# Optimization experiments

Measured on AMD Instinct MI355X. Metric: run time of the kernel, lower is better.

Reference implementation:

```python
import math
import jax, jax.numpy as jnp
import numpy as np

NQ = 4   # n_qubits
NL = 2   # n_layers
H = 16   # num_heads


def _apply_gate(state, gate, q, batched):
    """Apply a 1-qubit gate on wire q to batched state [N, 2**NQ]."""
    n = state.shape[0]
    left, right = 2 ** q, 2 ** (NQ - 1 - q)
    s = state.reshape(n, left, 2, right)
    eq = 'nab,nlbr->nlar' if batched else 'ab,nlbr->nlar'
    return jnp.einsum(eq, gate, s).reshape(n, 2 ** NQ)


def _rot(phi, theta, omega):
    """PennyLane Rot(phi, theta, omega) = RZ(omega) RY(theta) RZ(phi), 2x2 unitary."""
    c = jnp.cos(theta / 2).astype(jnp.complex64)
    s = jnp.sin(theta / 2).astype(jnp.complex64)
    ep = jnp.exp(-0.5j * (phi + omega).astype(jnp.complex64))
    em = jnp.exp(0.5j * (phi - omega).astype(jnp.complex64))
    m00 = ep * c
    m01 = -em * s
    m10 = jnp.conj(em) * s
    m11 = jnp.conj(ep) * c
    return jnp.stack([jnp.stack([m00, m01]), jnp.stack([m10, m11])])


def _cnot01(state):
    """CNOT with control wire 0, target wire 1 on [N, 16]."""
    n = state.shape[0]
    s = state.reshape(n, 2, 2, 2 ** (NQ - 2))
    s = jnp.stack([s[:, 0], s[:, 1, ::-1]], axis=1)
    return s.reshape(n, 2 ** NQ)


def _quantum_block(inputs, params):
    """Analytic state-vector simulation of the PennyLane circuit.

    inputs: [N, NQ] rotation angles (AngleEmbedding, default RX).
    params: [NL, NQ, 3] Rot parameters.
    Returns [N, NQ] Pauli-Z expectation values.
    """
    n = inputs.shape[0]
    state = jnp.zeros((n, 2 ** NQ), jnp.complex64).at[:, 0].set(1.0)
    # AngleEmbedding: RX(inputs[:, q]) on wire q
    for q in range(NQ):
        a = inputs[:, q] * 0.5
        c = jnp.cos(a).astype(jnp.complex64)
        s = (-1j) * jnp.sin(a).astype(jnp.complex64)
        gate = jnp.stack([jnp.stack([c, s], -1), jnp.stack([s, c], -1)], -2)  # [N,2,2]
        state = _apply_gate(state, gate, q, batched=True)
    # Variational layers
    for l in range(NL):
        for q in range(NQ):
            g = _rot(params[l, q, 0], params[l, q, 1], params[l, q, 2])
            state = _apply_gate(state, g, q, batched=False)
        state = _cnot01(state)
    probs = (jnp.abs(state) ** 2).reshape(n, 2, 2, 2, 2)
    z = jnp.array([1.0, -1.0], probs.dtype)
    letters = 'abcd'
    evs = [jnp.einsum(f'nabcd,{letters[i]}->n', probs, z) for i in range(NQ)]
    return jnp.stack(evs, axis=-1)


def reference(x, params, w_q, w_k, w_v, w_o):
    B, S, E = x.shape
    dk = E // H

    def proj(w):
        return (x @ w.T).reshape(B, S, H, dk).transpose(0, 2, 1, 3)  # [B,H,S,dk]

    q, k, v = proj(w_q), proj(w_k), proj(w_v)

    def inject(t):
        ang = t[..., :NQ].reshape(-1, NQ)
        ev = _quantum_block(ang, params).reshape(B, H, S, NQ).astype(t.dtype)
        return t.at[..., :NQ].set(ev)

    q, k, v = inject(q), inject(k), inject(v)
    scores = jnp.einsum('bhqd,bhkd->bhqk', q, k) / math.sqrt(dk)
    attn = jax.nn.softmax(scores, axis=-1)
    out = jnp.einsum('bhqk,bhkd->bhqd', attn, v)
    out = out.transpose(0, 2, 1, 3).reshape(B, S, E)
    return out @ w_o.T


def setup_inputs() -> dict:
    key = jax.random.key(0)
    ks = jax.random.split(key, 6)
    B, S, E = 2, 2048, 1024
    scale = 1.0 / math.sqrt(E)
    return {
        'x': jax.random.normal(ks[0], (B, S, E), jnp.float32),
        'params': jax.random.normal(ks[1], (NL, NQ, 3), jnp.float32),
        'w_q': jax.random.normal(ks[2], (E, E), jnp.float32) * scale,
        'w_k': jax.random.normal(ks[3], (E, E), jnp.float32) * scale,
        'w_v': jax.random.normal(ks[4], (E, E), jnp.float32) * scale,
        'w_o': jax.random.normal(ks[5], (E, E), jnp.float32) * scale,
    }
```

## Files before the change

### kernel.cpp

```cpp
#include <hip/hip_runtime.h>
#include <math.h>

#define BATCH 2
#define S_LEN 2048
#define E_DIM 1024
#define NHEAD 16
#define DK 64
#define NROWS (BATCH * S_LEN)

typedef _Float16 f16x8 __attribute__((ext_vector_type(8)));
typedef _Float16 f16x4 __attribute__((ext_vector_type(4)));
typedef float    f32x4 __attribute__((ext_vector_type(4)));

__global__ __launch_bounds__(256) void conv_all(
    const float* __restrict__ x,  const float* __restrict__ wq,
    const float* __restrict__ wk, const float* __restrict__ wv,
    const float* __restrict__ wo,
    _Float16* __restrict__ xh,  _Float16* __restrict__ wqh,
    _Float16* __restrict__ wkh, _Float16* __restrict__ wvh,
    _Float16* __restrict__ woh) {
    const int id = blockIdx.x;
    const float* src; _Float16* dst; int lid;
    if (id < 4096)      { src = x;  dst = xh;  lid = id; }
    else if (id < 5120) { src = wq; dst = wqh; lid = id - 4096; }
    else if (id < 6144) { src = wk; dst = wkh; lid = id - 5120; }
    else if (id < 7168) { src = wv; dst = wvh; lid = id - 6144; }
    else                { src = wo; dst = woh; lid = id - 7168; }
    const int i = lid * 256 + threadIdx.x;
    float4 v = ((const float4*)src)[i];
    f16x4 h;
    h[0] = (_Float16)v.x; h[1] = (_Float16)v.y;
    h[2] = (_Float16)v.z; h[3] = (_Float16)v.w;
    ((f16x4*)dst)[i] = h;
}

__device__ __forceinline__ void gemm_body(const _Float16* __restrict__ X,
                                          const _Float16* __restrict__ W,
                                          void* __restrict__ dstv, int mode,
                                          _Float16* smem) {
    _Float16* Xs = smem;
    _Float16* Ws = smem + 128 * 72;

    const int tid  = threadIdx.x;
    const int lane = tid & 63;
    const int wv   = tid >> 6;
    const int wy = wv >> 1, wx = wv & 1;
    const int l15 = lane & 15, quad = lane >> 4;
    const int m0 = blockIdx.y * 128, c0 = blockIdx.x * 128;

    const int srow = tid >> 3;
    const int skc  = (tid & 7) * 8;

    f32x4 acc[4][4];
#pragma unroll
    for (int i = 0; i < 4; ++i)
#pragma unroll
        for (int j = 0; j < 4; ++j) acc[i][j] = 0.f;

    for (int k0 = 0; k0 < E_DIM; k0 += 64) {
        f16x8 xg[4], wg[4];
#pragma unroll
        for (int c = 0; c < 4; ++c) {
            const int row = c * 32 + srow;
            xg[c] = *(const f16x8*)(X + (size_t)(m0 + row) * E_DIM + k0 + skc);
            wg[c] = *(const f16x8*)(W + (size_t)(c0 + row) * E_DIM + k0 + skc);
        }
        __syncthreads();
#pragma unroll
        for (int c = 0; c < 4; ++c) {
            const int row = c * 32 + srow;
            *(f16x8*)&Xs[row * 72 + skc] = xg[c];
            *(f16x8*)&Ws[row * 72 + skc] = wg[c];
        }
        __syncthreads();
#pragma unroll
        for (int ks = 0; ks < 2; ++ks) {
            f16x8 af[4], bf[4];
#pragma unroll
            for (int i = 0; i < 4; ++i) {
                af[i] = *(const f16x8*)&Xs[(wy * 64 + i * 16 + l15) * 72 + ks * 32 + quad * 8];
                bf[i] = *(const f16x8*)&Ws[(wx * 64 + i * 16 + l15) * 72 + ks * 32 + quad * 8];
            }
#pragma unroll
            for (int i = 0; i < 4; ++i)
#pragma unroll
                for (int j = 0; j < 4; ++j)
                    acc[i][j] = __builtin_amdgcn_mfma_f32_16x16x32_f16(af[i], bf[j], acc[i][j], 0, 0, 0);
        }
    }

    if (mode == 2) {
        __syncthreads();
        _Float16* Ct = smem;
#pragma unroll
        for (int i = 0; i < 4; ++i)
#pragma unroll
            for (int j = 0; j < 4; ++j) {
                const int col  = wx * 64 + j * 16 + l15;
                const int rowb = wy * 64 + i * 16 + quad * 4;
                f16x4 pk;
#pragma unroll
                for (int r = 0; r < 4; ++r) pk[r] = (_Float16)acc[i][j][r];
                *(f16x4*)&Ct[col * 136 + rowb] = pk;
            }
        __syncthreads();
        const int b  = m0 >> 11;
        const int s0 = m0 & 2047;
#pragma unroll
        for (int it = 0; it < 8; ++it) {
            const int c   = it * 256 + tid;
            const int col = c >> 4;
            const int rc  = c & 15;
            f16x8 v = *(const f16x8*)&Ct[col * 136 + rc * 8];
            const int e = c0 + col, h = e >> 6, d = e & 63;
            *(f16x8*)((_Float16*)dstv + ((size_t)((b * NHEAD + h) * DK + d)) * S_LEN + s0 + rc * 8) = v;
        }
        return;
    }

#pragma unroll
    for (int i = 0; i < 4; ++i)
#pragma unroll
        for (int j = 0; j < 4; ++j)
#pragma unroll
            for (int r = 0; r < 4; ++r) {
                const int row = m0 + wy * 64 + i * 16 + quad * 4 + r;
                const int col = c0 + wx * 64 + j * 16 + l15;
                if (mode == 0) {
                    ((float*)dstv)[(size_t)row * E_DIM + col] = acc[i][j][r];
                } else {
                    const int b = row >> 11, s = row & 2047;
                    const int h = col >> 6,  d = col & 63;
                    ((_Float16*)dstv)[(((size_t)(b * NHEAD + h) * S_LEN + s) * DK) + d] =
                        (_Float16)acc[i][j][r];
                }
            }
}

__global__ __launch_bounds__(256) void gemm_qkv(
    const _Float16* __restrict__ X,
    const _Float16* __restrict__ WQ, const _Float16* __restrict__ WK,
    const _Float16* __restrict__ WV,
    _Float16* __restrict__ Qh, _Float16* __restrict__ Kh,
    _Float16* __restrict__ VTh) {
    __shared__ __align__(16) _Float16 smem[2 * 128 * 72];
    const int z = blockIdx.z;
    const _Float16* W = (z == 0) ? WQ : (z == 1) ? WK : WV;
    void* dst = (z == 0) ? (void*)Qh : (z == 1) ? (void*)Kh : (void*)VTh;
    gemm_body(X, W, dst, (z == 2) ? 2 : 1, smem);
}

__global__ __launch_bounds__(256) void gemm_out(const _Float16* __restrict__ X,
                                                const _Float16* __restrict__ W,
                                                float* __restrict__ dst) {
    __shared__ __align__(16) _Float16 smem[2 * 128 * 72];
    gemm_body(X, W, dst, 0, smem);
}

__device__ __forceinline__ void apply_gate(float ar[16], float ai[16], int stride,
                                           float g00r, float g00i, float g01r, float g01i,
                                           float g10r, float g10i, float g11r, float g11i) {
#pragma unroll
    for (int i0 = 0; i0 < 16; ++i0) {
        if (i0 & stride) continue;
        const int i1 = i0 + stride;
        const float s0r = ar[i0], s0i = ai[i0];
        const float s1r = ar[i1], s1i = ai[i1];
        ar[i0] = g00r * s0r - g00i * s0i + g01r * s1r - g01i * s1i;
        ai[i0] = g00r * s0i + g00i * s0r + g01r * s1i + g01i * s1r;
        ar[i1] = g10r * s0r - g10i * s0i + g11r * s1r - g11i * s1i;
        ai[i1] = g10r * s0i + g10i * s0r + g11r * s1i + g11i * s1r;
    }
}

__global__ __launch_bounds__(256) void quantum_inject(_Float16* __restrict__ Q,
                                                      _Float16* __restrict__ K,
                                                      _Float16* __restrict__ VT,
                                                      const float* __restrict__ params) {
    const int id = blockIdx.x * 256 + threadIdx.x;
    const int which = id >> 16;
    const int rem = id & 65535;

    float angv[4];
    _Float16* qkbase = nullptr;
    _Float16* vbase  = nullptr;
    if (which == 2) {
        const int bh = rem >> 11, s = rem & 2047;
        vbase = VT + ((size_t)bh * DK) * S_LEN + s;
#pragma unroll
        for (int d = 0; d < 4; ++d) angv[d] = (float)vbase[(size_t)d * S_LEN];
    } else {
        qkbase = (which == 0 ? Q : K) + (size_t)rem * DK;
        const f16x4 a4 = *(const f16x4*)qkbase;
#pragma unroll
        for (int d = 0; d < 4; ++d) angv[d] = (float)a4[d];
    }

    float ar[16], ai[16];
#pragma unroll
    for (int i = 0; i < 16; ++i) { ar[i] = 0.f; ai[i] = 0.f; }
    ar[0] = 1.f;

#pragma unroll
    for (int q = 0; q < 4; ++q) {
        float sh, ch;
        sincosf(0.5f * angv[q], &sh, &ch);
        apply_gate(ar, ai, 8 >> q, ch, 0.f, 0.f, -sh, 0.f, -sh, ch, 0.f);
    }

#pragma unroll
    for (int l = 0; l < 2; ++l) {
#pragma unroll
        for (int q = 0; q < 4; ++q) {
            const float* pp = params + (l * 4 + q) * 3;
            const float phi = pp[0], th = pp[1], om = pp[2];
            float st, ct, sa, ca, sb, cb;
            sincosf(0.5f * th, &st, &ct);
            sincosf(0.5f * (phi + om), &sa, &ca);
            sincosf(0.5f * (phi - om), &sb, &cb);
            apply_gate(ar, ai, 8 >> q,
                       ct * ca, -ct * sa,
                       -st * cb, -st * sb,
                       st * cb, -st * sb,
                       ct * ca, ct * sa);
        }
#pragma unroll
        for (int r = 0; r < 4; ++r) {
            float tr = ar[8 + r], ti = ai[8 + r];
            ar[8 + r] = ar[12 + r]; ai[8 + r] = ai[12 + r];
            ar[12 + r] = tr;        ai[12 + r] = ti;
        }
    }

    float ev[4] = {0.f, 0.f, 0.f, 0.f};
#pragma unroll
    for (int i = 0; i < 16; ++i) {
        const float p = ar[i] * ar[i] + ai[i] * ai[i];
        ev[0] += (i & 8) ? -p : p;
        ev[1] += (i & 4) ? -p : p;
        ev[2] += (i & 2) ? -p : p;
        ev[3] += (i & 1) ? -p : p;
    }
    if (which == 2) {
#pragma unroll
        for (int d = 0; d < 4; ++d) vbase[(size_t)d * S_LEN] = (_Float16)ev[d];
    } else {
        f16x4 o;
#pragma unroll
        for (int d = 0; d < 4; ++d) o[d] = (_Float16)ev[d];
        *(f16x4*)qkbase = o;
    }
}

__global__ __launch_bounds__(256, 2) void attn5(const _Float16* __restrict__ Q,
                                                const _Float16* __restrict__ K,
                                                const _Float16* __restrict__ VT,
                                                _Float16* __restrict__ ctx) {
    __shared__ __align__(16) _Float16 Ks[2][64][72];
    __shared__ __align__(16) _Float16 Vs[2][64][72];
    __shared__ __align__(16) _Float16 Pw[4][32][72];

    const int tid = threadIdx.x, lane = tid & 63, w = tid >> 6;
    const int l15 = lane & 15, quad = lane >> 4;
    const int bh = blockIdx.y;
    const int qbase = blockIdx.x * 128 + w * 32;

    const _Float16* Qb = Q  + (size_t)bh * S_LEN * DK;
    const _Float16* Kb = K  + (size_t)bh * S_LEN * DK;
    const _Float16* Vb = VT + (size_t)bh * DK * S_LEN;

    const int r0   = tid >> 3;
    const int col0 = (tid & 7) * 8;

    f16x8 bf[2][2];
#pragma unroll
    for (int qn = 0; qn < 2; ++qn)
#pragma unroll
        for (int ks = 0; ks < 2; ++ks)
            bf[qn][ks] = *(const f16x8*)(Qb + (size_t)(qbase + qn * 16 + l15) * DK + ks * 32 + quad * 8);

    f32x4 oacc[4][2];
#pragma unroll
    for (int dt = 0; dt < 4; ++dt)
#pragma unroll
        for (int qn = 0; qn < 2; ++qn) oacc[dt][qn] = 0.f;
    float lpart[2] = {0.f, 0.f};

    f16x8 gk0, gk1, gv0, gv1;
    gk0 = *(const f16x8*)(Kb + (size_t)r0 * DK + col0);
    gk1 = *(const f16x8*)(Kb + (size_t)(r0 + 32) * DK + col0);
    gv0 = *(const f16x8*)(Vb + (size_t)r0 * S_LEN + col0);
    gv1 = *(const f16x8*)(Vb + (size_t)(r0 + 32) * S_LEN + col0);
    *(f16x8*)&Ks[0][r0][col0]      = gk0;
    *(f16x8*)&Ks[0][r0 + 32][col0] = gk1;
    *(f16x8*)&Vs[0][r0][col0]      = gv0;
    *(f16x8*)&Vs[0][r0 + 32][col0] = gv1;
    __syncthreads();

    for (int t = 0; t < S_LEN / 64; ++t) {
        const int buf = t & 1;
        if (t < S_LEN / 64 - 1) {
            const int kt = (t + 1) * 64;
            gk0 = *(const f16x8*)(Kb + (size_t)(kt + r0) * DK + col0);
            gk1 = *(const f16x8*)(Kb + (size_t)(kt + r0 + 32) * DK + col0);
            gv0 = *(const f16x8*)(Vb + (size_t)r0 * S_LEN + kt + col0);
            gv1 = *(const f16x8*)(Vb + (size_t)(r0 + 32) * S_LEN + kt + col0);
        }

        f16x8 af[4][2], vt[4][2];
#pragma unroll
        for (int kc = 0; kc < 4; ++kc)
#pragma unroll
            for (int ks = 0; ks < 2; ++ks)
                af[kc][ks] = *(const f16x8*)&Ks[buf][kc * 16 + l15][ks * 32 + quad * 8];
#pragma unroll
        for (int dt = 0; dt < 4; ++dt)
#pragma unroll
            for (int kh = 0; kh < 2; ++kh)
                vt[dt][kh] = *(const f16x8*)&Vs[buf][dt * 16 + l15][kh * 32 + quad * 8];

#pragma unroll
        for (int kc = 0; kc < 4; ++kc)
#pragma unroll
            for (int qn = 0; qn < 2; ++qn) {
                f32x4 st = 0.f;
                st = __builtin_amdgcn_mfma_f32_16x16x32_f16(af[kc][0], bf[qn][0], st, 0, 0, 0);
                st = __builtin_amdgcn_mfma_f32_16x16x32_f16(af[kc][1], bf[qn][1], st, 0, 0, 0);
                f16x4 pk; float ps = 0.f;
#pragma unroll
                for (int r = 0; r < 4; ++r) {
                    const float p = __expf(fmaf(st[r], 0.125f, -3.0f));
                    ps += p;
                    pk[r] = (_Float16)p;
                }
                lpart[qn] += ps;
                *(f16x4*)&Pw[w][qn * 16 + l15][kc * 16 + quad * 4] = pk;
            }

        f16x8 pb[2][2];
#pragma unroll
        for (int qn = 0; qn < 2; ++qn)
#pragma unroll
            for (int kh = 0; kh < 2; ++kh)
                pb[qn][kh] = *(const f16x8*)&Pw[w][qn * 16 + l15][kh * 32 + quad * 8];
#pragma unroll
        for (int dt = 0; dt < 4; ++dt)
#pragma unroll
            for (int qn = 0; qn < 2; ++qn) {
                oacc[dt][qn] = __builtin_amdgcn_mfma_f32_16x16x32_f16(vt[dt][0], pb[qn][0], oacc[dt][qn], 0, 0, 0);
                oacc[dt][qn] = __builtin_amdgcn_mfma_f32_16x16x32_f16(vt[dt][1], pb[qn][1], oacc[dt][qn], 0, 0, 0);
            }

        if (t < S_LEN / 64 - 1) {
            __syncthreads();
            *(f16x8*)&Ks[buf ^ 1][r0][col0]      = gk0;
            *(f16x8*)&Ks[buf ^ 1][r0 + 32][col0] = gk1;
            *(f16x8*)&Vs[buf ^ 1][r0][col0]      = gv0;
            *(f16x8*)&Vs[buf ^ 1][r0 + 32][col0] = gv1;
            __syncthreads();
        }
    }

    float inv[2];
#pragma unroll
    for (int qn = 0; qn < 2; ++qn) {
        float l = lpart[qn];
        l += __shfl_xor(l, 16);
        l += __shfl_xor(l, 32);
        inv[qn] = 1.f / l;
    }

#pragma unroll
    for (int dt = 0; dt < 4; ++dt)
#pragma unroll
        for (int qn = 0; qn < 2; ++qn) {
            f16x4 ov;
#pragma unroll
            for (int r = 0; r < 4; ++r) ov[r] = (_Float16)(oacc[dt][qn][r] * inv[qn]);
            *(f16x4*)&Pw[w][qn * 16 + l15][dt * 16 + quad * 4] = ov;
        }

    const int b = bh >> 4, h = bh & 15;
#pragma unroll
    for (int i = 0; i < 4; ++i) {
        const int c = i * 64 + lane;
        const int row = c >> 3, c8 = c & 7;
        f16x8 v = *(const f16x8*)&Pw[w][row][c8 * 8];
        *(f16x8*)(ctx + (size_t)(b * S_LEN + qbase + row) * E_DIM + h * DK + c8 * 8) = v;
    }
}

extern "C" void kernel_launch(void* const* d_in, const int* in_sizes, int n_in,
                              void* d_out, int out_size, void* d_ws, size_t ws_size,
                              hipStream_t stream) {
    const float* x      = (const float*)d_in[0];
    const float* params = (const float*)d_in[1];
    const float* w_q    = (const float*)d_in[2];
    const float* w_k    = (const float*)d_in[3];
    const float* w_v    = (const float*)d_in[4];
    const float* w_o    = (const float*)d_in[5];
    float* out = (float*)d_out;

    const size_t TENS = (size_t)NROWS * E_DIM;
    const size_t WEL  = (size_t)E_DIM * E_DIM;
    _Float16* xh  = (_Float16*)d_ws;
    _Float16* wqh = xh  + TENS;
    _Float16* wkh = wqh + WEL;
    _Float16* wvh = wkh + WEL;
    _Float16* woh = wvh + WEL;
    _Float16* Qh  = woh + WEL;
    _Float16* Kh  = Qh  + TENS;
    _Float16* VTh = Kh  + TENS;
    _Float16* CTXh= VTh + TENS;

    dim3 blk(256);

    conv_all<<<dim3(8192), blk, 0, stream>>>(x, w_q, w_k, w_v, w_o,
                                             xh, wqh, wkh, wvh, woh);

    gemm_qkv<<<dim3(E_DIM / 128, NROWS / 128, 3), blk, 0, stream>>>(
        xh, wqh, wkh, wvh, Qh, Kh, VTh);

    quantum_inject<<<dim3(768), blk, 0, stream>>>(Qh, Kh, VTh, params);

    attn5<<<dim3(S_LEN / 128, BATCH * NHEAD), blk, 0, stream>>>(Qh, Kh, VTh, CTXh);

    gemm_out<<<dim3(E_DIM / 128, NROWS / 128), blk, 0, stream>>>(CTXh, woh, out);
}
```

Before: 219.4 us.

## Load GEMM and attention tiles directly into LDS with XOR-swizzled layout

Replaces the register-staged global-to-LDS copies in the GEMM body and the attention kernel with direct global_load_lds transfers, using an XOR swizzle on 16-byte chunks in place of row padding to avoid LDS bank conflicts. This removes the round trip through VGPRs and one barrier per attention iteration, and lowers register pressure so occupancy hints rise to 3 blocks per CU. The catch is that the GEMM no longer overlaps its global loads with compute (load then sync each k-step), and the direct-to-LDS path depends on exact lane-to-address mapping being correct.

```diff
diff --git a/kernel.cpp b/kernel.cpp
--- a/kernel.cpp
+++ b/kernel.cpp
@@ -11,6 +11,13 @@
 typedef _Float16 f16x8 __attribute__((ext_vector_type(8)));
 typedef _Float16 f16x4 __attribute__((ext_vector_type(4)));
 typedef float    f32x4 __attribute__((ext_vector_type(4)));
+
+__device__ __forceinline__ void glds16(_Float16* lds, const _Float16* g) {
+    __builtin_amdgcn_global_load_lds(
+        (const __attribute__((address_space(1))) unsigned int*)g,
+        (__attribute__((address_space(3))) unsigned int*)lds,
+        16, 0, 0);
+}
 
 __global__ __launch_bounds__(256) void conv_all(
     const float* __restrict__ x,  const float* __restrict__ wq,
@@ -39,17 +46,22 @@
                                           void* __restrict__ dstv, int mode,
                                           _Float16* smem) {
     _Float16* Xs = smem;
-    _Float16* Ws = smem + 128 * 72;
+    _Float16* Ws = smem + 128 * 64;
 
     const int tid  = threadIdx.x;
     const int lane = tid & 63;
-    const int wv   = tid >> 6;
-    const int wy = wv >> 1, wx = wv & 1;
+    const int w    = tid >> 6;
+    const int wy = w >> 1, wx = w & 1;
     const int l15 = lane & 15, quad = lane >> 4;
+    const int sw  = l15 & 7;
     const int m0 = blockIdx.y * 128, c0 = blockIdx.x * 128;
 
-    const int srow = tid >> 3;
-    const int skc  = (tid & 7) * 8;
+    const int lrow = lane >> 3;
+    const int gcol = ((lane & 7) ^ lrow) * 8;
+    const _Float16* xg = X + (size_t)(m0 + w * 32 + lrow) * E_DIM + gcol;
+    const _Float16* wg = W + (size_t)(c0 + w * 32 + lrow) * E_DIM + gcol;
+    _Float16* xls = Xs + (w * 32) * 64;
+    _Float16* wls = Ws + (w * 32) * 64;
 
     f32x4 acc[4][4];
 #pragma unroll
@@ -58,28 +70,23 @@
         for (int j = 0; j < 4; ++j) acc[i][j] = 0.f;
 
     for (int k0 = 0; k0 < E_DIM; k0 += 64) {
-        f16x8 xg[4], wg[4];
-#pragma unroll
-        for (int c = 0; c < 4; ++c) {
-            const int row = c * 32 + srow;
-            xg[c] = *(const f16x8*)(X + (size_t)(m0 + row) * E_DIM + k0 + skc);
-            wg[c] = *(const f16x8*)(W + (size_t)(c0 + row) * E_DIM + k0 + skc);
-        }
         __syncthreads();
 #pragma unroll
-        for (int c = 0; c < 4; ++c) {
-            const int row = c * 32 + srow;
-            *(f16x8*)&Xs[row * 72 + skc] = xg[c];
-            *(f16x8*)&Ws[row * 72 + skc] = wg[c];
-        }
+        for (int c = 0; c < 4; ++c)
+            glds16(xls + c * 512, xg + (size_t)c * 8 * E_DIM + k0);
+#pragma unroll
+        for (int c = 0; c < 4; ++c)
+            glds16(wls + c * 512, wg + (size_t)c * 8 * E_DIM + k0);
         __syncthreads();
+
 #pragma unroll
         for (int ks = 0; ks < 2; ++ks) {
             f16x8 af[4], bf[4];
 #pragma unroll
             for (int i = 0; i < 4; ++i) {
-                af[i] = *(const f16x8*)&Xs[(wy * 64 + i * 16 + l15) * 72 + ks * 32 + quad * 8];
-                bf[i] = *(const f16x8*)&Ws[(wx * 64 + i * 16 + l15) * 72 + ks * 32 + quad * 8];
+                const int pc = ((ks * 4 + quad) ^ sw) * 8;
+                af[i] = *(const f16x8*)&Xs[(wy * 64 + i * 16 + l15) * 64 + pc];
+                bf[i] = *(const f16x8*)&Ws[(wx * 64 + i * 16 + l15) * 64 + pc];
             }
 #pragma unroll
             for (int i = 0; i < 4; ++i)
@@ -137,23 +144,23 @@
             }
 }
 
-__global__ __launch_bounds__(256) void gemm_qkv(
+__global__ __launch_bounds__(256, 3) void gemm_qkv(
     const _Float16* __restrict__ X,
     const _Float16* __restrict__ WQ, const _Float16* __restrict__ WK,
     const _Float16* __restrict__ WV,
     _Float16* __restrict__ Qh, _Float16* __restrict__ Kh,
     _Float16* __restrict__ VTh) {
-    __shared__ __align__(16) _Float16 smem[2 * 128 * 72];
+    __shared__ __align__(16) _Float16 smem[128 * 136];
     const int z = blockIdx.z;
     const _Float16* W = (z == 0) ? WQ : (z == 1) ? WK : WV;
     void* dst = (z == 0) ? (void*)Qh : (z == 1) ? (void*)Kh : (void*)VTh;
     gemm_body(X, W, dst, (z == 2) ? 2 : 1, smem);
 }
 
-__global__ __launch_bounds__(256) void gemm_out(const _Float16* __restrict__ X,
-                                                const _Float16* __restrict__ W,
-                                                float* __restrict__ dst) {
-    __shared__ __align__(16) _Float16 smem[2 * 128 * 72];
+__global__ __launch_bounds__(256, 3) void gemm_out(const _Float16* __restrict__ X,
+                                                   const _Float16* __restrict__ W,
+                                                   float* __restrict__ dst) {
+    __shared__ __align__(16) _Float16 smem[128 * 136];
     gemm_body(X, W, dst, 0, smem);
 }
 
@@ -252,16 +259,16 @@
     }
 }
 
-__global__ __launch_bounds__(256, 2) void attn5(const _Float16* __restrict__ Q,
+__global__ __launch_bounds__(256, 3) void attn6(const _Float16* __restrict__ Q,
                                                 const _Float16* __restrict__ K,
                                                 const _Float16* __restrict__ VT,
                                                 _Float16* __restrict__ ctx) {
-    __shared__ __align__(16) _Float16 Ks[2][64][72];
-    __shared__ __align__(16) _Float16 Vs[2][64][72];
-    __shared__ __align__(16) _Float16 Pw[4][32][72];
+    __shared__ __align__(16) _Float16 KVs[2][2][64 * 64];
+    __shared__ __align__(16) _Float16 Pw[4][32 * 72];
 
     const int tid = threadIdx.x, lane = tid & 63, w = tid >> 6;
     const int l15 = lane & 15, quad = lane >> 4;
+    const int sw  = l15 & 7;
     const int bh = blockIdx.y;
     const int qbase = blockIdx.x * 128 + w * 32;
 
@@ -269,8 +276,10 @@
     const _Float16* Kb = K  + (size_t)bh * S_LEN * DK;
     const _Float16* Vb = VT + (size_t)bh * DK * S_LEN;
 
-    const int r0   = tid >> 3;
-    const int col0 = (tid & 7) * 8;
+    const int lrow = lane >> 3;
+    const int gcol = ((lane & 7) ^ lrow) * 8;
+    const _Float16* kg = Kb + (size_t)(w * 16 + lrow) * DK + gcol;
+    const _Float16* vg = Vb + (size_t)(w * 16 + lrow) * S_LEN + gcol;
 
     f16x8 bf[2][2];
 #pragma unroll
@@ -286,25 +295,24 @@
         for (int qn = 0; qn < 2; ++qn) oacc[dt][qn] = 0.f;
     float lpart[2] = {0.f, 0.f};
 
-    f16x8 gk0, gk1, gv0, gv1;
-    gk0 = *(const f16x8*)(Kb + (size_t)r0 * DK + col0);
-    gk1 = *(const f16x8*)(Kb + (size_t)(r0 + 32) * DK + col0);
-    gv0 = *(const f16x8*)(Vb + (size_t)r0 * S_LEN + col0);
-    gv1 = *(const f16x8*)(Vb + (size_t)(r0 + 32) * S_LEN + col0);
-    *(f16x8*)&Ks[0][r0][col0]      = gk0;
-    *(f16x8*)&Ks[0][r0 + 32][col0] = gk1;
-    *(f16x8*)&Vs[0][r0][col0]      = gv0;
-    *(f16x8*)&Vs[0][r0 + 32][col0] = gv1;
+#pragma unroll
+    for (int c = 0; c < 2; ++c) {
+        glds16(&KVs[0][0][(w * 16 + c * 8) * 64], kg + (size_t)(c * 8) * DK);
+        glds16(&KVs[0][1][(w * 16 + c * 8) * 64], vg + (size_t)(c * 8) * S_LEN);
+    }
     __syncthreads();
 
     for (int t = 0; t < S_LEN / 64; ++t) {
         const int buf = t & 1;
         if (t < S_LEN / 64 - 1) {
             const int kt = (t + 1) * 64;
-            gk0 = *(const f16x8*)(Kb + (size_t)(kt + r0) * DK + col0);
-            gk1 = *(const f16x8*)(Kb + (size_t)(kt + r0 + 32) * DK + col0);
-            gv0 = *(const f16x8*)(Vb + (size_t)r0 * S_LEN + kt + col0);
-            gv1 = *(const f16x8*)(Vb + (size_t)(r0 + 32) * S_LEN + kt + col0);
+#pragma unroll
+            for (int c = 0; c < 2; ++c) {
+                glds16(&KVs[buf ^ 1][0][(w * 16 + c * 8) * 64],
+                       kg + (size_t)(kt + c * 8) * DK);
+                glds16(&KVs[buf ^ 1][1][(w * 16 + c * 8) * 64],
+                       vg + (size_t)(c * 8) * S_LEN + kt);
+            }
         }
 
         f16x8 af[4][2], vt[4][2];
@@ -312,12 +320,12 @@
         for (int kc = 0; kc < 4; ++kc)
 #pragma unroll
             for (int ks = 0; ks < 2; ++ks)
-                af[kc][ks] = *(const f16x8*)&Ks[buf][kc * 16 + l15][ks * 32 + quad * 8];
+                af[kc][ks] = *(const f16x8*)&KVs[buf][0][(kc * 16 + l15) * 64 + ((ks * 4 + quad) ^ sw) * 8];
 #pragma unroll
         for (int dt = 0; dt < 4; ++dt)
 #pragma unroll
             for (int kh = 0; kh < 2; ++kh)
-                vt[dt][kh] = *(const f16x8*)&Vs[buf][dt * 16 + l15][kh * 32 + quad * 8];
+                vt[dt][kh] = *(const f16x8*)&KVs[buf][1][(dt * 16 + l15) * 64 + ((kh * 4 + quad) ^ sw) * 8];
 
 #pragma unroll
         for (int kc = 0; kc < 4; ++kc)
@@ -334,7 +342,7 @@
                     pk[r] = (_Float16)p;
                 }
                 lpart[qn] += ps;
-                *(f16x4*)&Pw[w][qn * 16 + l15][kc * 16 + quad * 4] = pk;
+                *(f16x4*)&Pw[w][(qn * 16 + l15) * 72 + kc * 16 + quad * 4] = pk;
             }
 
         f16x8 pb[2][2];
@@ -342,7 +350,7 @@
         for (int qn = 0; qn < 2; ++qn)
 #pragma unroll
             for (int kh = 0; kh < 2; ++kh)
-                pb[qn][kh] = *(const f16x8*)&Pw[w][qn * 16 + l15][kh * 32 + quad * 8];
+                pb[qn][kh] = *(const f16x8*)&Pw[w][(qn * 16 + l15) * 72 + kh * 32 + quad * 8];
 #pragma unroll
         for (int dt = 0; dt < 4; ++dt)
 #pragma unroll
@@ -351,14 +359,7 @@
                 oacc[dt][qn] = __builtin_amdgcn_mfma_f32_16x16x32_f16(vt[dt][1], pb[qn][1], oacc[dt][qn], 0, 0, 0);
             }
 
-        if (t < S_LEN / 64 - 1) {
-            __syncthreads();
-            *(f16x8*)&Ks[buf ^ 1][r0][col0]      = gk0;
-            *(f16x8*)&Ks[buf ^ 1][r0 + 32][col0] = gk1;
-            *(f16x8*)&Vs[buf ^ 1][r0][col0]      = gv0;
-            *(f16x8*)&Vs[buf ^ 1][r0 + 32][col0] = gv1;
-            __syncthreads();
-        }
+        __syncthreads();
     }
 
     float inv[2];
@@ -377,7 +378,7 @@
             f16x4 ov;
 #pragma unroll
             for (int r = 0; r < 4; ++r) ov[r] = (_Float16)(oacc[dt][qn][r] * inv[qn]);
-            *(f16x4*)&Pw[w][qn * 16 + l15][dt * 16 + quad * 4] = ov;
+            *(f16x4*)&Pw[w][(qn * 16 + l15) * 72 + dt * 16 + quad * 4] = ov;
         }
 
     const int b = bh >> 4, h = bh & 15;
@@ -385,7 +386,7 @@
     for (int i = 0; i < 4; ++i) {
         const int c = i * 64 + lane;
         const int row = c >> 3, c8 = c & 7;
-        f16x8 v = *(const f16x8*)&Pw[w][row][c8 * 8];
+        f16x8 v = *(const f16x8*)&Pw[w][row * 72 + c8 * 8];
         *(f16x8*)(ctx + (size_t)(b * S_LEN + qbase + row) * E_DIM + h * DK + c8 * 8) = v;
     }
 }
@@ -423,7 +424,7 @@
 
     quantum_inject<<<dim3(768), blk, 0, stream>>>(Qh, Kh, VTh, params);
 
-    attn5<<<dim3(S_LEN / 128, BATCH * NHEAD), blk, 0, stream>>>(Qh, Kh, VTh, CTXh);
+    attn6<<<dim3(S_LEN / 128, BATCH * NHEAD), blk, 0, stream>>>(Qh, Kh, VTh, CTXh);
 
     gemm_out<<<dim3(E_DIM / 128, NROWS / 128), blk, 0, stream>>>(CTXh, woh, out);
 }
```

Measured after the change: 215.3 us. About the same (-1.9%).
